# Kernel tuning notes

Measured on AMD Instinct MI355X. Metric: run time of the kernel, lower is better.

## Reference

```python
import jax, jax.numpy as jnp
import numpy as np

N = 8192
IN_F = 512
OUT_F = 256
EDGE_P = 0.02  # adjacency density


def setup_inputs() -> dict:
    key = jax.random.key(0)
    k1, k2, k3, k4 = jax.random.split(key, 4)
    x = jax.random.normal(k1, (N, IN_F), dtype=jnp.float32)
    # xavier_uniform with gain=1.414 ~ std gain*sqrt(2/(fan_in+fan_out))
    W = jax.random.normal(k2, (IN_F, OUT_F), dtype=jnp.float32) * (1.414 * np.sqrt(2.0 / (IN_F + OUT_F)))
    a = jax.random.normal(k3, (2 * OUT_F, 1), dtype=jnp.float32) * (1.414 * np.sqrt(2.0 / (2 * OUT_F + 1)))
    adj = (jax.random.uniform(k4, (N, N)) < EDGE_P).astype(jnp.float32)
    return {"x": x, "adj": adj, "W": W, "a": a}


def reference(x, adj, W, a):
    h = x @ W                        # [N, F]
    F = h.shape[1]
    # repeat/cat reduces to an outer sum of two [N] vectors.
    s_src = (h @ a[:F]).squeeze(-1)  # [N], contribution of h_i
    s_dst = (h @ a[F:]).squeeze(-1)  # [N], contribution of h_j
    e = jax.nn.leaky_relu(s_src[:, None] + s_dst[None, :], negative_slope=0.2)  # [N, N]
    # NOTE: original code softmaxes over the FULL row, THEN multiplies by adj.
    attention = jax.nn.softmax(e, axis=1) * adj  # [N, N]
    h_prime = attention @ h                      # [N, F]
    return h_prime, attention
```

## Files before the change

### kernel.cpp

```cpp
#include <hip/hip_runtime.h>
#include <hip/hip_bf16.h>

#define N_NODES 8192
#define IN_F    512
#define OUT_F   256
#define MAXNZ   512

typedef float v4f  __attribute__((ext_vector_type(4)));
typedef __attribute__((ext_vector_type(8)))  short bf16x8;
typedef __attribute__((ext_vector_type(16))) float f32x16;
typedef unsigned short u16;
typedef unsigned int   u32;

__device__ __forceinline__ u16 f2bf(float f) {
  u32 u = __float_as_uint(f);
  u += 0x7fffu + ((u >> 16) & 1u);
  return (u16)(u >> 16);
}
__device__ __forceinline__ float bf2f(u16 h) {
  return __uint_as_float(((u32)h) << 16);
}

__global__ __launch_bounds__(256) void k_cast_x(const float* __restrict__ x,
                                                u16* __restrict__ x_hi,
                                                u16* __restrict__ x_lo) {
  const int idx = blockIdx.x * 256 + threadIdx.x;
  const float4 v = ((const float4*)x)[idx];
  u16 h0 = f2bf(v.x), h1 = f2bf(v.y), h2 = f2bf(v.z), h3 = f2bf(v.w);
  u16 l0 = f2bf(v.x - bf2f(h0)), l1 = f2bf(v.y - bf2f(h1));
  u16 l2 = f2bf(v.z - bf2f(h2)), l3 = f2bf(v.w - bf2f(h3));
  uint2 hp, lp;
  hp.x = (u32)h0 | ((u32)h1 << 16); hp.y = (u32)h2 | ((u32)h3 << 16);
  lp.x = (u32)l0 | ((u32)l1 << 16); lp.y = (u32)l2 | ((u32)l3 << 16);
  ((uint2*)x_hi)[idx] = hp;
  ((uint2*)x_lo)[idx] = lp;
}

__global__ __launch_bounds__(256) void k_cast_wt(const float* __restrict__ W,
                                                 u16* __restrict__ wt_hi,
                                                 u16* __restrict__ wt_lo) {
  const int k = blockIdx.x;
  const int n = threadIdx.x;
  const float v = W[(size_t)k * OUT_F + n];
  const u16 h = f2bf(v);
  wt_hi[(size_t)n * IN_F + k] = h;
  wt_lo[(size_t)n * IN_F + k] = f2bf(v - bf2f(h));
}

#define GBK 64
__global__ __launch_bounds__(256) void k_gemm_mfma(const u16* __restrict__ x_hi,
                                                   const u16* __restrict__ x_lo,
                                                   const u16* __restrict__ wt_hi,
                                                   const u16* __restrict__ wt_lo,
                                                   const float* __restrict__ a,
                                                   u16* __restrict__ h_bf,
                                                   float* __restrict__ s_src,
                                                   float* __restrict__ s_dst) {
  __shared__ u16 As_hi[64 * 68], As_lo[64 * 68], Bs_hi[64 * 68], Bs_lo[64 * 68];
  const int t    = threadIdx.x;
  const int bn   = blockIdx.x & 3;
  const int bm   = blockIdx.x >> 2;
  const int m0   = bm * 64, n0 = bn * 64;
  const int lane = t & 63;
  const int w    = t >> 6;
  const int wm   = w & 1, wn = w >> 1;

  const int sm = t >> 2;
  const int sk = (t & 3) * 16;

  f32x16 acc = {};

  for (int k0 = 0; k0 < IN_F; k0 += GBK) {
#pragma unroll
    for (int i = 0; i < 2; ++i) {
      const int ko = sk + i * 8;
      *(bf16x8*)&As_hi[sm * 68 + ko] = *(const bf16x8*)&x_hi[(size_t)(m0 + sm) * IN_F + k0 + ko];
      *(bf16x8*)&As_lo[sm * 68 + ko] = *(const bf16x8*)&x_lo[(size_t)(m0 + sm) * IN_F + k0 + ko];
      *(bf16x8*)&Bs_hi[sm * 68 + ko] = *(const bf16x8*)&wt_hi[(size_t)(n0 + sm) * IN_F + k0 + ko];
      *(bf16x8*)&Bs_lo[sm * 68 + ko] = *(const bf16x8*)&wt_lo[(size_t)(n0 + sm) * IN_F + k0 + ko];
    }
    __syncthreads();
    const int am  = wm * 32 + (lane & 31);
    const int bn_ = wn * 32 + (lane & 31);
#pragma unroll
    for (int kk = 0; kk < 4; ++kk) {
      const int ko = kk * 16 + (lane >> 5) * 8;
      const bf16x8 ah = *(const bf16x8*)&As_hi[am * 68 + ko];
      const bf16x8 al = *(const bf16x8*)&As_lo[am * 68 + ko];
      const bf16x8 bh = *(const bf16x8*)&Bs_hi[bn_ * 68 + ko];
      const bf16x8 bl = *(const bf16x8*)&Bs_lo[bn_ * 68 + ko];
      acc = __builtin_amdgcn_mfma_f32_32x32x16_bf16(ah, bh, acc, 0, 0, 0);
      acc = __builtin_amdgcn_mfma_f32_32x32x16_bf16(al, bh, acc, 0, 0, 0);
      acc = __builtin_amdgcn_mfma_f32_32x32x16_bf16(ah, bl, acc, 0, 0, 0);
    }
    __syncthreads();
  }
  const int colg = n0 + wn * 32 + (lane & 31);
  const float asv = a[colg];
  const float adv = a[OUT_F + colg];
#pragma unroll
  for (int r = 0; r < 16; ++r) {
    const int row = m0 + wm * 32 + (r & 3) + 8 * (r >> 2) + 4 * (lane >> 5);
    const float v = acc[r];
    h_bf[(size_t)row * OUT_F + colg] = f2bf(v);
    float vs = v * asv, vd = v * adv;
#pragma unroll
    for (int off = 1; off < 32; off <<= 1) {
      vs += __shfl_xor(vs, off);
      vd += __shfl_xor(vd, off);
    }
    if ((lane & 31) == 0) {
      atomicAdd(&s_src[row], vs);
      atomicAdd(&s_dst[row], vd);
    }
  }
}

__device__ __forceinline__ float lrelu_exp(float v) {
  const float e = v > 0.f ? v : 0.2f * v;
  return __expf(e);
}

__global__ __launch_bounds__(256) void k_attn(const float* __restrict__ adj,
                                              const u16* __restrict__ h_bf,
                                              const float* __restrict__ s_src,
                                              const float* __restrict__ s_dst,
                                              float* __restrict__ out_hp,
                                              float* __restrict__ out_att) {
  __shared__ float nza[MAXNZ];
  __shared__ int   nzj[MAXNZ];
  __shared__ float redbuf[4];
  __shared__ int   cnt;

  const int t = threadIdx.x;
  const int i = blockIdx.x;
  const float ssrc = s_src[i];
  if (t == 0) cnt = 0;

  const float4* sd4 = (const float4*)s_dst;
  float4 p[8];
  float lsum = 0.f;
#pragma unroll
  for (int c = 0; c < 8; ++c) {
    const float4 s = sd4[c * 256 + t];
    p[c].x = lrelu_exp(ssrc + s.x);
    p[c].y = lrelu_exp(ssrc + s.y);
    p[c].z = lrelu_exp(ssrc + s.z);
    p[c].w = lrelu_exp(ssrc + s.w);
    lsum += p[c].x + p[c].y + p[c].z + p[c].w;
  }
#pragma unroll
  for (int off = 32; off > 0; off >>= 1) lsum += __shfl_down(lsum, off);
  if ((t & 63) == 0) redbuf[t >> 6] = lsum;
  __syncthreads();
  const float inv = 1.0f / (redbuf[0] + redbuf[1] + redbuf[2] + redbuf[3]);

  const v4f* adj4 = (const v4f*)(adj + (size_t)i * N_NODES);
  v4f*       att4 = (v4f*)(out_att + (size_t)i * N_NODES);
  v4f av[8];
#pragma unroll
  for (int c = 0; c < 8; ++c) av[c] = __builtin_nontemporal_load(adj4 + c * 256 + t);
#pragma unroll
  for (int c = 0; c < 8; ++c) {
    v4f att;
    att.x = av[c].x * (p[c].x * inv);
    att.y = av[c].y * (p[c].y * inv);
    att.z = av[c].z * (p[c].z * inv);
    att.w = av[c].w * (p[c].w * inv);
    __builtin_nontemporal_store(att, att4 + c * 256 + t);
    const int j = (c * 256 + t) * 4;
    if (av[c].x != 0.f) { const int k = atomicAdd(&cnt, 1); if (k < MAXNZ) { nzj[k] = j + 0; nza[k] = att.x; } }
    if (av[c].y != 0.f) { const int k = atomicAdd(&cnt, 1); if (k < MAXNZ) { nzj[k] = j + 1; nza[k] = att.y; } }
    if (av[c].z != 0.f) { const int k = atomicAdd(&cnt, 1); if (k < MAXNZ) { nzj[k] = j + 2; nza[k] = att.z; } }
    if (av[c].w != 0.f) { const int k = atomicAdd(&cnt, 1); if (k < MAXNZ) { nzj[k] = j + 3; nza[k] = att.w; } }
  }
  __syncthreads();

  const int n = cnt < MAXNZ ? cnt : MAXNZ;
  float acc = 0.f;
#pragma unroll 8
  for (int k = 0; k < n; ++k) {
    acc = fmaf(nza[k], bf2f(h_bf[(size_t)nzj[k] * OUT_F + t]), acc);
  }
  out_hp[(size_t)i * OUT_F + t] = acc;
}

extern "C" void kernel_launch(void* const* d_in, const int* in_sizes, int n_in,
                              void* d_out, int out_size, void* d_ws, size_t ws_size,
                              hipStream_t stream) {
  const float* x   = (const float*)d_in[0];
  const float* adj = (const float*)d_in[1];
  const float* W   = (const float*)d_in[2];
  const float* a   = (const float*)d_in[3];

  float* out_hp  = (float*)d_out;
  float* out_att = (float*)d_out + (size_t)N_NODES * OUT_F;

  char* ws = (char*)d_ws;
  float* ssrc_ws = (float*)ws;                       ws += N_NODES * 4;
  float* sdst_ws = (float*)ws;                       ws += N_NODES * 4;
  u16*   x_hi    = (u16*)ws;                         ws += (size_t)N_NODES * IN_F * 2;
  u16*   x_lo    = (u16*)ws;                         ws += (size_t)N_NODES * IN_F * 2;
  u16*   wt_hi   = (u16*)ws;                         ws += (size_t)OUT_F * IN_F * 2;
  u16*   wt_lo   = (u16*)ws;                         ws += (size_t)OUT_F * IN_F * 2;
  u16*   h_bf    = (u16*)ws;                         ws += (size_t)N_NODES * OUT_F * 2;

  hipMemsetAsync(ssrc_ws, 0, 2 * N_NODES * sizeof(float), stream);

  k_cast_x<<<(N_NODES * IN_F / 4) / 256, 256, 0, stream>>>(x, x_hi, x_lo);
  k_cast_wt<<<IN_F, OUT_F, 0, stream>>>(W, wt_hi, wt_lo);
  k_gemm_mfma<<<(N_NODES / 64) * (OUT_F / 64), 256, 0, stream>>>(
      x_hi, x_lo, wt_hi, wt_lo, a, h_bf, ssrc_ws, sdst_ws);
  k_attn<<<N_NODES, 256, 0, stream>>>(adj, h_bf, ssrc_ws, sdst_ws, out_hp, out_att);
}
```

Baseline: 512.7 us.

## Fuse x bf16 split into GEMM, swizzle blocks, hoist adj loads

Removes the separate x cast kernel and its hi/lo workspace by splitting fp32 x into bf16 hi/lo while staging tiles inside the GEMM. Remaps block indices so that blocks sharing x rows run close together for L2 reuse. In the attention kernel, the adjacency row loads are issued before the softmax-sum computation to overlap memory latency. The trade-off is that the split conversion is now done redundantly by each of the 4 column blocks, at the cost of more ALU work and more registers.

```diff
diff --git a/kernel.cpp b/kernel.cpp
--- a/kernel.cpp
+++ b/kernel.cpp
@@ -19,21 +19,6 @@
 }
 __device__ __forceinline__ float bf2f(u16 h) {
   return __uint_as_float(((u32)h) << 16);
-}
-
-__global__ __launch_bounds__(256) void k_cast_x(const float* __restrict__ x,
-                                                u16* __restrict__ x_hi,
-                                                u16* __restrict__ x_lo) {
-  const int idx = blockIdx.x * 256 + threadIdx.x;
-  const float4 v = ((const float4*)x)[idx];
-  u16 h0 = f2bf(v.x), h1 = f2bf(v.y), h2 = f2bf(v.z), h3 = f2bf(v.w);
-  u16 l0 = f2bf(v.x - bf2f(h0)), l1 = f2bf(v.y - bf2f(h1));
-  u16 l2 = f2bf(v.z - bf2f(h2)), l3 = f2bf(v.w - bf2f(h3));
-  uint2 hp, lp;
-  hp.x = (u32)h0 | ((u32)h1 << 16); hp.y = (u32)h2 | ((u32)h3 << 16);
-  lp.x = (u32)l0 | ((u32)l1 << 16); lp.y = (u32)l2 | ((u32)l3 << 16);
-  ((uint2*)x_hi)[idx] = hp;
-  ((uint2*)x_lo)[idx] = lp;
 }
 
 __global__ __launch_bounds__(256) void k_cast_wt(const float* __restrict__ W,
@@ -48,8 +33,12 @@
 }
 
 #define GBK 64
-__global__ __launch_bounds__(256) void k_gemm_mfma(const u16* __restrict__ x_hi,
-                                                   const u16* __restrict__ x_lo,
+
+#define SPLIT1(F, Hu, Lu, J) { const u16 hh = f2bf(F); Hu.s[J] = hh; Lu.s[J] = f2bf(F - bf2f(hh)); }
+#define SPLIT4(V, Hu, Lu) { SPLIT1(V.x, Hu, Lu, 0); SPLIT1(V.y, Hu, Lu, 1); \
+                            SPLIT1(V.z, Hu, Lu, 2); SPLIT1(V.w, Hu, Lu, 3); }
+
+__global__ __launch_bounds__(256) void k_gemm_mfma(const float* __restrict__ x,
                                                    const u16* __restrict__ wt_hi,
                                                    const u16* __restrict__ wt_lo,
                                                    const float* __restrict__ a,
@@ -58,8 +47,9 @@
                                                    float* __restrict__ s_dst) {
   __shared__ u16 As_hi[64 * 68], As_lo[64 * 68], Bs_hi[64 * 68], Bs_lo[64 * 68];
   const int t    = threadIdx.x;
-  const int bn   = blockIdx.x & 3;
-  const int bm   = blockIdx.x >> 2;
+  const int id2  = (blockIdx.x & 7) * 64 + (blockIdx.x >> 3);
+  const int bn   = id2 & 3;
+  const int bm   = id2 >> 2;
   const int m0   = bm * 64, n0 = bn * 64;
   const int lane = t & 63;
   const int w    = t >> 6;
@@ -71,11 +61,27 @@
   f32x16 acc = {};
 
   for (int k0 = 0; k0 < IN_F; k0 += GBK) {
+    const float4* xp = (const float4*)&x[(size_t)(m0 + sm) * IN_F + k0 + sk];
+    const float4 f0 = xp[0], f1 = xp[1], f2 = xp[2], f3 = xp[3];
+    union { bf16x8 v; u16 s[8]; } Ha, La, Hb, Lb;
+    { union { bf16x8 v; struct { u16 s0,s1,s2,s3,s4,s5,s6,s7; }; } dummy; (void)dummy; }
+    SPLIT4(f0, Ha, La);
+    { const u16 h4 = f2bf(f1.x); Ha.s[4] = h4; La.s[4] = f2bf(f1.x - bf2f(h4)); }
+    { const u16 h5 = f2bf(f1.y); Ha.s[5] = h5; La.s[5] = f2bf(f1.y - bf2f(h5)); }
+    { const u16 h6 = f2bf(f1.z); Ha.s[6] = h6; La.s[6] = f2bf(f1.z - bf2f(h6)); }
+    { const u16 h7 = f2bf(f1.w); Ha.s[7] = h7; La.s[7] = f2bf(f1.w - bf2f(h7)); }
+    SPLIT4(f2, Hb, Lb);
+    { const u16 h4 = f2bf(f3.x); Hb.s[4] = h4; Lb.s[4] = f2bf(f3.x - bf2f(h4)); }
+    { const u16 h5 = f2bf(f3.y); Hb.s[5] = h5; Lb.s[5] = f2bf(f3.y - bf2f(h5)); }
+    { const u16 h6 = f2bf(f3.z); Hb.s[6] = h6; Lb.s[6] = f2bf(f3.z - bf2f(h6)); }
+    { const u16 h7 = f2bf(f3.w); Hb.s[7] = h7; Lb.s[7] = f2bf(f3.w - bf2f(h7)); }
+    *(bf16x8*)&As_hi[sm * 68 + sk]     = Ha.v;
+    *(bf16x8*)&As_lo[sm * 68 + sk]     = La.v;
+    *(bf16x8*)&As_hi[sm * 68 + sk + 8] = Hb.v;
+    *(bf16x8*)&As_lo[sm * 68 + sk + 8] = Lb.v;
 #pragma unroll
     for (int i = 0; i < 2; ++i) {
       const int ko = sk + i * 8;
-      *(bf16x8*)&As_hi[sm * 68 + ko] = *(const bf16x8*)&x_hi[(size_t)(m0 + sm) * IN_F + k0 + ko];
-      *(bf16x8*)&As_lo[sm * 68 + ko] = *(const bf16x8*)&x_lo[(size_t)(m0 + sm) * IN_F + k0 + ko];
       *(bf16x8*)&Bs_hi[sm * 68 + ko] = *(const bf16x8*)&wt_hi[(size_t)(n0 + sm) * IN_F + k0 + ko];
       *(bf16x8*)&Bs_lo[sm * 68 + ko] = *(const bf16x8*)&wt_lo[(size_t)(n0 + sm) * IN_F + k0 + ko];
     }
@@ -134,8 +140,14 @@
 
   const int t = threadIdx.x;
   const int i = blockIdx.x;
+  if (t == 0) cnt = 0;
+
+  const v4f* adj4 = (const v4f*)(adj + (size_t)i * N_NODES);
+  v4f av[8];
+#pragma unroll
+  for (int c = 0; c < 8; ++c) av[c] = __builtin_nontemporal_load(adj4 + c * 256 + t);
+
   const float ssrc = s_src[i];
-  if (t == 0) cnt = 0;
 
   const float4* sd4 = (const float4*)s_dst;
   float4 p[8];
@@ -155,11 +167,7 @@
   __syncthreads();
   const float inv = 1.0f / (redbuf[0] + redbuf[1] + redbuf[2] + redbuf[3]);
 
-  const v4f* adj4 = (const v4f*)(adj + (size_t)i * N_NODES);
-  v4f*       att4 = (v4f*)(out_att + (size_t)i * N_NODES);
-  v4f av[8];
-#pragma unroll
-  for (int c = 0; c < 8; ++c) av[c] = __builtin_nontemporal_load(adj4 + c * 256 + t);
+  v4f* att4 = (v4f*)(out_att + (size_t)i * N_NODES);
 #pragma unroll
   for (int c = 0; c < 8; ++c) {
     v4f att;
@@ -199,17 +207,14 @@
   char* ws = (char*)d_ws;
   float* ssrc_ws = (float*)ws;                       ws += N_NODES * 4;
   float* sdst_ws = (float*)ws;                       ws += N_NODES * 4;
-  u16*   x_hi    = (u16*)ws;                         ws += (size_t)N_NODES * IN_F * 2;
-  u16*   x_lo    = (u16*)ws;                         ws += (size_t)N_NODES * IN_F * 2;
   u16*   wt_hi   = (u16*)ws;                         ws += (size_t)OUT_F * IN_F * 2;
   u16*   wt_lo   = (u16*)ws;                         ws += (size_t)OUT_F * IN_F * 2;
   u16*   h_bf    = (u16*)ws;                         ws += (size_t)N_NODES * OUT_F * 2;
 
   hipMemsetAsync(ssrc_ws, 0, 2 * N_NODES * sizeof(float), stream);
 
-  k_cast_x<<<(N_NODES * IN_F / 4) / 256, 256, 0, stream>>>(x, x_hi, x_lo);
   k_cast_wt<<<IN_F, OUT_F, 0, stream>>>(W, wt_hi, wt_lo);
   k_gemm_mfma<<<(N_NODES / 64) * (OUT_F / 64), 256, 0, stream>>>(
-      x_hi, x_lo, wt_hi, wt_lo, a, h_bf, ssrc_ws, sdst_ws);
+      x, wt_hi, wt_lo, a, h_bf, ssrc_ws, sdst_ws);
   k_attn<<<N_NODES, 256, 0, stream>>>(adj, h_bf, ssrc_ws, sdst_ws, out_hp, out_att);
 }
```

Result: no change. 506.2 us (-1.3%).
